# Kernel optimization log

Measured on AMD Instinct MI355X. Metric: run time of the kernel, lower is better.

The kernel has to match this reference:

```python
import jax, jax.numpy as jnp
import numpy as np

DIMS = 2048
HEAD_DIM = 64
NUM_HEADS = DIMS // HEAD_DIM   # 32
GQA_HEADS = 2                  # KV heads
EPS = 1e-8


def setup_inputs() -> dict:
    key = jax.random.key(0)
    ks = jax.random.split(key, 6)
    b, s = 2, 2048
    kv_dims = HEAD_DIM * GQA_HEADS  # 128
    x = jax.random.normal(ks[0], (b, s, DIMS), dtype=jnp.float32)
    Wq = jax.random.normal(ks[1], (DIMS, DIMS), dtype=jnp.float32) * 0.02
    Wk = jax.random.normal(ks[2], (kv_dims, DIMS), dtype=jnp.float32) * 0.02
    Wv = jax.random.normal(ks[3], (kv_dims, DIMS), dtype=jnp.float32) * 0.02
    Wo = jax.random.normal(ks[4], (DIMS, DIMS), dtype=jnp.float32) * 0.02
    norm_scale = jnp.ones((DIMS,), dtype=jnp.float32)           # RMSNorm.scale
    split_scale = jnp.full((DIMS,), 0.1, dtype=jnp.float32)     # RMS_split.scale
    return {"x": x, "norm_scale": norm_scale, "split_scale": split_scale,
            "Wq": Wq, "Wk": Wk, "Wv": Wv, "Wo": Wo}


def reference(x, norm_scale, split_scale, Wq, Wk, Wv, Wo):
    b, s, d = x.shape
    H, G, dh = NUM_HEADS, GQA_HEADS, HEAD_DIM
    hpg = H // G  # query heads per KV group

    # RMS_split pre-norm: RMSNorm (l2-norm based) then elementwise scale
    nrm = jnp.linalg.norm(x, axis=-1, keepdims=True) * (d ** -0.5)
    h = (norm_scale * x / (nrm + EPS)) * split_scale

    # projections (nn.Linear with weight [out, in], no bias)
    q = (h @ Wq.T).reshape(b, s, H, dh)          # b s H dh
    k = (h @ Wk.T).reshape(b, s, G, dh)          # b s G dh
    v = (h @ Wv.T).reshape(b, s, G, dh)

    # group query heads: b G hpg s dh
    q = q.transpose(0, 2, 1, 3).reshape(b, G, hpg, s, dh)
    k = k.transpose(0, 2, 1, 3)                  # b G s dh
    v = v.transpose(0, 2, 1, 3)                  # b G s dh

    scores = jnp.einsum('bghsd,bgtd->bghst', q, k) / np.float32(np.sqrt(dh))
    attn = jax.nn.softmax(scores, axis=-1)
    out = jnp.einsum('bghst,bgtd->bghsd', attn, v)   # b G hpg s dh

    out = out.reshape(b, H, s, dh).transpose(0, 2, 1, 3).reshape(b, s, H * dh)
    return x + out @ Wo.T
```

## Files before the change

### kernel.cpp

```cpp
#include <hip/hip_runtime.h>

typedef unsigned short u16;
typedef unsigned int u32;
typedef __bf16 bf16x8 __attribute__((ext_vector_type(8)));
typedef float f32x4 __attribute__((ext_vector_type(4)));

#define DIMS 2048
#define SEQ 2048
#define BATCH 2
#define NH 32
#define NG 2
#define DH 64
#define MROWS (BATCH * SEQ)
#define KVD (NG * DH)

#define SCL2 (0.125f * 1.44269504088896f)

__device__ __forceinline__ u16 f2bf(float f) {
  u32 u = __float_as_uint(f);
  u32 r = u + 0x7fffu + ((u >> 16) & 1u);
  return (u16)(r >> 16);
}
__device__ __forceinline__ u32 pack2(float a, float b) {
  return (u32)f2bf(a) | ((u32)f2bf(b) << 16);
}
__device__ __forceinline__ u32 cvtpk(float a, float b) {
#if __has_builtin(__builtin_amdgcn_cvt_pk_bf16_f32)
  typedef __bf16 bf16x2 __attribute__((ext_vector_type(2)));
  union {
    bf16x2 v;
    u32 u;
  } r;
  r.v = __builtin_amdgcn_cvt_pk_bf16_f32(a, b);
  return r.u;
#else
  return pack2(a, b);
#endif
}
__device__ __forceinline__ void glds16(const u16* g, u16* l) {
  __builtin_amdgcn_global_load_lds(
      (const __attribute__((address_space(1))) void*)g,
      (__attribute__((address_space(3))) void*)l, 16, 0, 0);
}

__global__ __launch_bounds__(256) void rms_split_kernel(
    const float* __restrict__ x, const float* __restrict__ ns,
    const float* __restrict__ ss, u16* __restrict__ h) {
  const int row = blockIdx.x;
  const int tid = threadIdx.x;
  const float* xr = x + (size_t)row * DIMS;
  float4 v0 = ((const float4*)xr)[tid];
  float4 v1 = ((const float4*)xr)[tid + 256];
  float s = v0.x * v0.x + v0.y * v0.y + v0.z * v0.z + v0.w * v0.w +
            v1.x * v1.x + v1.y * v1.y + v1.z * v1.z + v1.w * v1.w;
#pragma unroll
  for (int d = 1; d < 64; d <<= 1) s += __shfl_xor(s, d, 64);
  __shared__ float red[4];
  if ((tid & 63) == 0) red[tid >> 6] = s;
  __syncthreads();
  float tot = red[0] + red[1] + red[2] + red[3];
  float inv = 1.0f / (sqrtf(tot * (1.0f / DIMS)) + 1e-8f);
  float4 a0 = ((const float4*)ns)[tid];
  float4 a1 = ((const float4*)ns)[tid + 256];
  float4 b0 = ((const float4*)ss)[tid];
  float4 b1 = ((const float4*)ss)[tid + 256];
  uint2 o0, o1;
  o0.x = pack2(v0.x * a0.x * b0.x * inv, v0.y * a0.y * b0.y * inv);
  o0.y = pack2(v0.z * a0.z * b0.z * inv, v0.w * a0.w * b0.w * inv);
  o1.x = pack2(v1.x * a1.x * b1.x * inv, v1.y * a1.y * b1.y * inv);
  o1.y = pack2(v1.z * a1.z * b1.z * inv, v1.w * a1.w * b1.w * inv);
  uint2* hr = (uint2*)(h + (size_t)row * DIMS);
  hr[tid] = o0;
  hr[tid + 256] = o1;
}

__global__ __launch_bounds__(256) void cvt2_kernel(const float* __restrict__ a,
                                                   u16* __restrict__ oa,
                                                   const float* __restrict__ b,
                                                   u16* __restrict__ ob,
                                                   int half) {
  const int bx = blockIdx.x;
  const float* src = bx < half ? a : b;
  u16* dst = bx < half ? oa : ob;
  const int i = (bx < half ? bx : bx - half) * 256 + threadIdx.x;
  float4 v = ((const float4*)src)[i];
  uint2 r;
  r.x = pack2(v.x, v.y);
  r.y = pack2(v.z, v.w);
  ((uint2*)dst)[i] = r;
}

template <int MODE>
__global__ __launch_bounds__(256) void gemm_bt(
    const u16* __restrict__ A, const u16* __restrict__ B, void* __restrict__ Cv,
    const float* __restrict__ R, u16* __restrict__ kb, u16* __restrict__ vtb,
    int M, int N, int K) {
  __shared__ u16 As[128 * 32];
  __shared__ u16 Bs[128 * 32];
  const int tid = threadIdx.x;
  const int lane = tid & 63;
  const int wv = tid >> 6;
  const int fr = lane & 15;
  const int fq = lane >> 4;
  const int m0 = blockIdx.y * 128;
  const int n0 = blockIdx.x * 128;
  const int wm = wv & 1;
  const int wn = wv >> 1;

  const int srow = tid >> 2;
  const int scol = (tid & 3) * 8;
  const u16* Ag0 = A + (size_t)(m0 + srow) * K + scol;
  const u16* Ag1 = A + (size_t)(m0 + srow + 64) * K + scol;
  const u16* Bg0 = B + (size_t)(n0 + srow) * K + scol;
  const u16* Bg1 = B + (size_t)(n0 + srow + 64) * K + scol;
  u16* Al0 = As + wv * 512;
  u16* Al1 = As + 2048 + wv * 512;
  u16* Bl0 = Bs + wv * 512;
  u16* Bl1 = Bs + 2048 + wv * 512;

  f32x4 acc[4][4];
#pragma unroll
  for (int i = 0; i < 4; ++i)
#pragma unroll
    for (int j = 0; j < 4; ++j)
#pragma unroll
      for (int e = 0; e < 4; ++e) acc[i][j][e] = 0.0f;

  const u16* ap[4];
  const u16* bp[4];
#pragma unroll
  for (int i = 0; i < 4; ++i) {
    ap[i] = As + (wm * 64 + i * 16 + fr) * 32 + fq * 8;
    bp[i] = Bs + (wn * 64 + i * 16 + fr) * 32 + fq * 8;
  }

  for (int k0 = 0; k0 < K; k0 += 32) {
    glds16(Ag0 + k0, Al0);
    glds16(Ag1 + k0, Al1);
    glds16(Bg0 + k0, Bl0);
    glds16(Bg1 + k0, Bl1);
    __syncthreads();
    bf16x8 af[4], bf[4];
#pragma unroll
    for (int i = 0; i < 4; ++i) {
      af[i] = *(const bf16x8*)ap[i];
      bf[i] = *(const bf16x8*)bp[i];
    }
#pragma unroll
    for (int i = 0; i < 4; ++i)
#pragma unroll
      for (int j = 0; j < 4; ++j)
        acc[i][j] = __builtin_amdgcn_mfma_f32_16x16x32_bf16(af[i], bf[j],
                                                            acc[i][j], 0, 0, 0);
    __syncthreads();
  }

#pragma unroll
  for (int i = 0; i < 4; ++i) {
    const int m = m0 + wm * 64 + i * 16 + fq * 4;
#pragma unroll
    for (int j = 0; j < 4; ++j) {
      const int n = n0 + wn * 64 + j * 16 + fr;
#pragma unroll
      for (int r = 0; r < 4; ++r) {
        if (MODE == 1) {
          const size_t idx = (size_t)(m + r) * N + n;
          ((float*)Cv)[idx] = R[idx] + acc[i][j][r];
        } else {
          if (n0 < 2048) {
            ((u16*)Cv)[(size_t)(m + r) * DIMS + n] = f2bf(acc[i][j][r]);
          } else {
            const int token = m + r;
            const int bb = token >> 11;
            const int srw = token & 2047;
            const int t = srw >> 6;
            const int rowin = srw & 63;
            if (n0 < 2176) {
              const int d = n - 2048;
              const int gg = d >> 6;
              const int dd = d & 63;
              const int c = ((dd >> 5) << 2) | ((dd >> 3) & 3);
              const int jj = dd & 7;
              const int pos = (rowin & 32) | ((rowin & 4) << 2) |
                              ((rowin & 0x18) >> 1) | (rowin & 3);
              kb[(((size_t)(bb * NG + gg) * 32 + t) * 8 + c) * 512 + pos * 8 +
                 jj] = f2bf(acc[i][j][r] * SCL2);
            } else {
              const int d = n - 2176;
              const int gg = d >> 6;
              const int dv = d & 63;
              const int c = rowin >> 3;
              const int jj = rowin & 7;
              vtb[(((size_t)(bb * NG + gg) * 32 + t) * 8 + c) * 512 + dv * 8 +
                  jj] = f2bf(acc[i][j][r]);
            }
          }
        }
      }
    }
  }
}

__global__ __launch_bounds__(256, 4) void attn_kernel(
    const u16* __restrict__ q, const u16* __restrict__ kbuf,
    const u16* __restrict__ vT, u16* __restrict__ out) {
  __shared__ u16 Ks[2][8 * 512];
  __shared__ u16 Vs[2][8 * 512];
  const int tid = threadIdx.x;
  const int lane = tid & 63;
  const int wv = tid >> 6;
  const int fr = lane & 15;
  const int fq = lane >> 4;
  const int b = blockIdx.x >> 5;
  const int hq = blockIdx.x & 31;
  const int g = hq >> 4;
  const int q0 = blockIdx.y * 128 + wv * 32;

  bf16x8 af[2][2];
#pragma unroll
  for (int mt = 0; mt < 2; ++mt)
#pragma unroll
    for (int kx = 0; kx < 2; ++kx)
      af[mt][kx] =
          *(const bf16x8*)(q + (size_t)(b * SEQ + q0 + mt * 16 + fr) * DIMS +
                           hq * DH + kx * 32 + fq * 8);

  f32x4 Oa[2][4];
  f32x4 On[2];
#pragma unroll
  for (int mt = 0; mt < 2; ++mt) {
#pragma unroll
    for (int e = 0; e < 4; ++e) On[mt][e] = 0.0f;
#pragma unroll
    for (int j = 0; j < 4; ++j)
#pragma unroll
      for (int e = 0; e < 4; ++e) Oa[mt][j][e] = 0.0f;
  }

  bf16x8 onev;
#pragma unroll
  for (int e = 0; e < 8; ++e) onev[e] = (__bf16)1.0f;

  const u16* ksrc = kbuf + (size_t)(b * NG + g) * 32 * 4096;
  const u16* vsrc = vT + (size_t)(b * NG + g) * 32 * 4096;

  const int c0 = wv * 2;
#define STAGE(buf, tile)                                     \
  {                                                          \
    const size_t tb_ = (size_t)(tile)*4096;                  \
    _Pragma("unroll") for (int s = 0; s < 2; ++s) {          \
      const int c = c0 + s;                                  \
      glds16(ksrc + tb_ + c * 512 + lane * 8, &Ks[buf][c * 512]); \
      glds16(vsrc + tb_ + c * 512 + lane * 8, &Vs[buf][c * 512]); \
    }                                                        \
  }

#define COMPUTE(buf)                                                          \
  {                                                                           \
    _Pragma("unroll") for (int kg = 0; kg < 2; ++kg) {                        \
      bf16x8 kf00 = *(const bf16x8*)(&Ks[buf][fq * 512 + (kg * 32 + fr) * 8]); \
      bf16x8 kf01 =                                                           \
          *(const bf16x8*)(&Ks[buf][(4 + fq) * 512 + (kg * 32 + fr) * 8]);    \
      bf16x8 kf10 =                                                           \
          *(const bf16x8*)(&Ks[buf][fq * 512 + (kg * 32 + 16 + fr) * 8]);     \
      bf16x8 kf11 = *(const bf16x8*)(&Ks[buf][(4 + fq) * 512 +                \
                                              (kg * 32 + 16 + fr) * 8]);      \
      bf16x8 vf[4];                                                           \
      _Pragma("unroll") for (int jt = 0; jt < 4; ++jt) vf[jt] =               \
          *(const bf16x8*)(&Vs[buf][(kg * 4 + fq) * 512 + (jt * 16 + fr) * 8]); \
      _Pragma("unroll") for (int mt = 0; mt < 2; ++mt) {                      \
        f32x4 s0 = {0.0f, 0.0f, 0.0f, 0.0f};                                  \
        f32x4 s1 = {0.0f, 0.0f, 0.0f, 0.0f};                                  \
        s0 = __builtin_amdgcn_mfma_f32_16x16x32_bf16(kf00, af[mt][0], s0, 0,  \
                                                     0, 0);                   \
        s0 = __builtin_amdgcn_mfma_f32_16x16x32_bf16(kf01, af[mt][1], s0, 0,  \
                                                     0, 0);                   \
        s1 = __builtin_amdgcn_mfma_f32_16x16x32_bf16(kf10, af[mt][0], s1, 0,  \
                                                     0, 0);                   \
        s1 = __builtin_amdgcn_mfma_f32_16x16x32_bf16(kf11, af[mt][1], s1, 0,  \
                                                     0, 0);                   \
        const float p0 = __builtin_amdgcn_exp2f(s0[0]);                       \
        const float p1 = __builtin_amdgcn_exp2f(s0[1]);                       \
        const float p2 = __builtin_amdgcn_exp2f(s0[2]);                       \
        const float p3 = __builtin_amdgcn_exp2f(s0[3]);                       \
        const float p4 = __builtin_amdgcn_exp2f(s1[0]);                       \
        const float p5 = __builtin_amdgcn_exp2f(s1[1]);                       \
        const float p6 = __builtin_amdgcn_exp2f(s1[2]);                       \
        const float p7 = __builtin_amdgcn_exp2f(s1[3]);                       \
        union {                                                               \
          bf16x8 v;                                                           \
          u32 u[4];                                                           \
        } pu;                                                                 \
        pu.u[0] = cvtpk(p0, p1);                                              \
        pu.u[1] = cvtpk(p2, p3);                                              \
        pu.u[2] = cvtpk(p4, p5);                                              \
        pu.u[3] = cvtpk(p6, p7);                                              \
        _Pragma("unroll") for (int jt = 0; jt < 4; ++jt) Oa[mt][jt] =         \
            __builtin_amdgcn_mfma_f32_16x16x32_bf16(pu.v, vf[jt], Oa[mt][jt], \
                                                    0, 0, 0);                 \
        On[mt] = __builtin_amdgcn_mfma_f32_16x16x32_bf16(pu.v, onev, On[mt],  \
                                                         0, 0, 0);            \
      }                                                                       \
    }                                                                         \
  }

  STAGE(0, 0);
  for (int it = 0; it < 32; it += 2) {
    STAGE(1, (it + 1) & 31);
    asm volatile("s_waitcnt vmcnt(4)\ns_barrier" ::: "memory");
    COMPUTE(0);
    asm volatile("s_barrier" ::: "memory");
    STAGE(0, (it + 2) & 31);
    asm volatile("s_waitcnt vmcnt(4)\ns_barrier" ::: "memory");
    COMPUTE(1);
    asm volatile("s_barrier" ::: "memory");
  }
#undef STAGE
#undef COMPUTE

#pragma unroll
  for (int mt = 0; mt < 2; ++mt)
#pragma unroll
    for (int r = 0; r < 4; ++r) {
      const float invl = 1.0f / On[mt][r];
      const int row = q0 + mt * 16 + fq * 4 + r;
#pragma unroll
      for (int jt = 0; jt < 4; ++jt)
        out[(size_t)(b * SEQ + row) * DIMS + hq * DH + jt * 16 + fr] =
            f2bf(Oa[mt][jt][r] * invl);
    }
}

extern "C" void kernel_launch(void* const* d_in, const int* in_sizes, int n_in,
                              void* d_out, int out_size, void* d_ws,
                              size_t ws_size, hipStream_t stream) {
  const float* x = (const float*)d_in[0];
  const float* ns = (const float*)d_in[1];
  const float* ssc = (const float*)d_in[2];
  const float* Wq = (const float*)d_in[3];
  const float* Wk = (const float*)d_in[4];
  const float* Wv = (const float*)d_in[5];
  const float* Wo = (const float*)d_in[6];

  char* ws = (char*)d_ws;
  u16* hbuf = (u16*)(ws);
  u16* bqkv = (u16*)(ws + 16777216);
  u16* bWo = (u16*)(ws + 26214400);
  u16* qb = (u16*)(ws + 34603008);
  u16* kb = (u16*)(ws + 51380224);
  u16* vtb = (u16*)(ws + 52428800);
  u16* ab = (u16*)(ws + 53477376);

  rms_split_kernel<<<dim3(4096), dim3(256), 0, stream>>>(x, ns, ssc, hbuf);
  cvt2_kernel<<<dim3(8192), dim3(256), 0, stream>>>(Wq, bqkv, Wo, bWo, 4096);
  cvt2_kernel<<<dim3(512), dim3(256), 0, stream>>>(
      Wk, bqkv + (size_t)2048 * 2048, Wv, bqkv + (size_t)2176 * 2048, 256);

  gemm_bt<2><<<dim3(18, 32), dim3(256), 0, stream>>>(
      hbuf, bqkv, qb, nullptr, kb, vtb, 4096, 2048, 2048);
  attn_kernel<<<dim3(64, 16), dim3(256), 0, stream>>>(qb, kb, vtb, ab);
  gemm_bt<1><<<dim3(16, 32), dim3(256), 0, stream>>>(
      ab, bWo, d_out, x, nullptr, nullptr, 4096, 2048, 2048);
}
```

Baseline: 331.0 us.

## Double-buffer GEMM LDS tiles and merge weight conversion kernels into one

The bf16 GEMM now keeps two LDS buffers for the A and B tiles. It issues the global-to-LDS loads for the next K slice before computing the current one, and uses partial vmcnt waits with raw barriers so memory latency overlaps the MFMA work. The two fp32-to-bf16 weight conversion launches are also merged into a single launch, saving one kernel launch. The cost is double the LDS per block, which may lower occupancy, plus hand-written waitcnt/barrier assembly that has to match the exact number of outstanding loads.

```diff
diff --git a/kernel.cpp b/kernel.cpp
--- a/kernel.cpp
+++ b/kernel.cpp
@@ -74,20 +74,29 @@
   hr[tid + 256] = o1;
 }
 
-__global__ __launch_bounds__(256) void cvt2_kernel(const float* __restrict__ a,
-                                                   u16* __restrict__ oa,
-                                                   const float* __restrict__ b,
-                                                   u16* __restrict__ ob,
-                                                   int half) {
+__global__ __launch_bounds__(256) void cvt4_kernel(
+    const float* __restrict__ Wq, const float* __restrict__ Wo,
+    const float* __restrict__ Wk, const float* __restrict__ Wv,
+    u16* __restrict__ bqkv, u16* __restrict__ bWo) {
   const int bx = blockIdx.x;
-  const float* src = bx < half ? a : b;
-  u16* dst = bx < half ? oa : ob;
-  const int i = (bx < half ? bx : bx - half) * 256 + threadIdx.x;
-  float4 v = ((const float4*)src)[i];
+  const float* src;
+  u16* dst;
+  int i;
+  if (bx < 4096) {
+    src = Wq; dst = bqkv; i = bx;
+  } else if (bx < 8192) {
+    src = Wo; dst = bWo; i = bx - 4096;
+  } else if (bx < 8448) {
+    src = Wk; dst = bqkv + (size_t)2048 * 2048; i = bx - 8192;
+  } else {
+    src = Wv; dst = bqkv + (size_t)2176 * 2048; i = bx - 8448;
+  }
+  const int idx = i * 256 + threadIdx.x;
+  float4 v = ((const float4*)src)[idx];
   uint2 r;
   r.x = pack2(v.x, v.y);
   r.y = pack2(v.z, v.w);
-  ((uint2*)dst)[i] = r;
+  ((uint2*)dst)[idx] = r;
 }
 
 template <int MODE>
@@ -95,8 +104,8 @@
     const u16* __restrict__ A, const u16* __restrict__ B, void* __restrict__ Cv,
     const float* __restrict__ R, u16* __restrict__ kb, u16* __restrict__ vtb,
     int M, int N, int K) {
-  __shared__ u16 As[128 * 32];
-  __shared__ u16 Bs[128 * 32];
+  __shared__ u16 As[2][128 * 32];
+  __shared__ u16 Bs[2][128 * 32];
   const int tid = threadIdx.x;
   const int lane = tid & 63;
   const int wv = tid >> 6;
@@ -113,10 +122,6 @@
   const u16* Ag1 = A + (size_t)(m0 + srow + 64) * K + scol;
   const u16* Bg0 = B + (size_t)(n0 + srow) * K + scol;
   const u16* Bg1 = B + (size_t)(n0 + srow + 64) * K + scol;
-  u16* Al0 = As + wv * 512;
-  u16* Al1 = As + 2048 + wv * 512;
-  u16* Bl0 = Bs + wv * 512;
-  u16* Bl1 = Bs + 2048 + wv * 512;
 
   f32x4 acc[4][4];
 #pragma unroll
@@ -126,34 +131,49 @@
 #pragma unroll
       for (int e = 0; e < 4; ++e) acc[i][j][e] = 0.0f;
 
-  const u16* ap[4];
-  const u16* bp[4];
-#pragma unroll
-  for (int i = 0; i < 4; ++i) {
-    ap[i] = As + (wm * 64 + i * 16 + fr) * 32 + fq * 8;
-    bp[i] = Bs + (wn * 64 + i * 16 + fr) * 32 + fq * 8;
-  }
-
-  for (int k0 = 0; k0 < K; k0 += 32) {
-    glds16(Ag0 + k0, Al0);
-    glds16(Ag1 + k0, Al1);
-    glds16(Bg0 + k0, Bl0);
-    glds16(Bg1 + k0, Bl1);
-    __syncthreads();
-    bf16x8 af[4], bf[4];
-#pragma unroll
-    for (int i = 0; i < 4; ++i) {
-      af[i] = *(const bf16x8*)ap[i];
-      bf[i] = *(const bf16x8*)bp[i];
-    }
-#pragma unroll
-    for (int i = 0; i < 4; ++i)
-#pragma unroll
-      for (int j = 0; j < 4; ++j)
-        acc[i][j] = __builtin_amdgcn_mfma_f32_16x16x32_bf16(af[i], bf[j],
-                                                            acc[i][j], 0, 0, 0);
-    __syncthreads();
-  }
+#define GSTAGE(buf, kk)                            \
+  {                                                \
+    glds16(Ag0 + (kk), &As[buf][wv * 512]);        \
+    glds16(Ag1 + (kk), &As[buf][2048 + wv * 512]); \
+    glds16(Bg0 + (kk), &Bs[buf][wv * 512]);        \
+    glds16(Bg1 + (kk), &Bs[buf][2048 + wv * 512]); \
+  }
+
+#define GCOMP(buf)                                                            \
+  {                                                                           \
+    bf16x8 af_[4], bf_[4];                                                    \
+    _Pragma("unroll") for (int i = 0; i < 4; ++i) {                           \
+      af_[i] = *(const bf16x8*)(&As[buf][(wm * 64 + i * 16 + fr) * 32 +       \
+                                         fq * 8]);                            \
+      bf_[i] = *(const bf16x8*)(&Bs[buf][(wn * 64 + i * 16 + fr) * 32 +       \
+                                         fq * 8]);                            \
+    }                                                                         \
+    _Pragma("unroll") for (int i = 0; i < 4; ++i)                             \
+        _Pragma("unroll") for (int j = 0; j < 4; ++j) acc[i][j] =             \
+        __builtin_amdgcn_mfma_f32_16x16x32_bf16(af_[i], bf_[j], acc[i][j], 0, \
+                                                0, 0);                        \
+  }
+
+  GSTAGE(0, 0);
+  int k0 = 0;
+  for (; k0 + 64 < K; k0 += 64) {
+    GSTAGE(1, k0 + 32);
+    asm volatile("s_waitcnt vmcnt(4)\ns_barrier" ::: "memory");
+    GCOMP(0);
+    asm volatile("s_barrier" ::: "memory");
+    GSTAGE(0, k0 + 64);
+    asm volatile("s_waitcnt vmcnt(4)\ns_barrier" ::: "memory");
+    GCOMP(1);
+    asm volatile("s_barrier" ::: "memory");
+  }
+  GSTAGE(1, k0 + 32);
+  asm volatile("s_waitcnt vmcnt(4)\ns_barrier" ::: "memory");
+  GCOMP(0);
+  asm volatile("s_barrier" ::: "memory");
+  asm volatile("s_waitcnt vmcnt(0)\ns_barrier" ::: "memory");
+  GCOMP(1);
+#undef GSTAGE
+#undef GCOMP
 
 #pragma unroll
   for (int i = 0; i < 4; ++i) {
@@ -245,14 +265,14 @@
   const u16* vsrc = vT + (size_t)(b * NG + g) * 32 * 4096;
 
   const int c0 = wv * 2;
-#define STAGE(buf, tile)                                     \
-  {                                                          \
-    const size_t tb_ = (size_t)(tile)*4096;                  \
-    _Pragma("unroll") for (int s = 0; s < 2; ++s) {          \
-      const int c = c0 + s;                                  \
+#define STAGE(buf, tile)                                          \
+  {                                                               \
+    const size_t tb_ = (size_t)(tile)*4096;                       \
+    _Pragma("unroll") for (int s = 0; s < 2; ++s) {               \
+      const int c = c0 + s;                                       \
       glds16(ksrc + tb_ + c * 512 + lane * 8, &Ks[buf][c * 512]); \
       glds16(vsrc + tb_ + c * 512 + lane * 8, &Vs[buf][c * 512]); \
-    }                                                        \
+    }                                                             \
   }
 
 #define COMPUTE(buf)                                                          \
@@ -352,9 +372,7 @@
   u16* ab = (u16*)(ws + 53477376);
 
   rms_split_kernel<<<dim3(4096), dim3(256), 0, stream>>>(x, ns, ssc, hbuf);
-  cvt2_kernel<<<dim3(8192), dim3(256), 0, stream>>>(Wq, bqkv, Wo, bWo, 4096);
-  cvt2_kernel<<<dim3(512), dim3(256), 0, stream>>>(
-      Wk, bqkv + (size_t)2048 * 2048, Wv, bqkv + (size_t)2176 * 2048, 256);
+  cvt4_kernel<<<dim3(8704), dim3(256), 0, stream>>>(Wq, Wo, Wk, Wv, bqkv, bWo);
 
   gemm_bt<2><<<dim3(18, 32), dim3(256), 0, stream>>>(
       hbuf, bqkv, qb, nullptr, kb, vtb, 4096, 2048, 2048);
```

New measurement: 299.8 us. 9.4% less time.
